# Performance work log

Measured on AMD Instinct MI355X. Metric: run time of the kernel, lower is better.

## Reference

```python
import jax, jax.numpy as jnp
import numpy as np

N, E = 20000, 100000          # nodes, edges
H = 64                        # node_hidden_dim (== node_input_dim)
EIN, EH = 16, 128             # edge_input_dim, edge_hidden_dim
STEPS = 3                     # num_steps


def setup_inputs() -> dict:
    key = jax.random.key(0)
    ks = jax.random.split(key, 10)
    s = 0.05
    return {
        "node_features": jax.random.normal(ks[0], (N, H), jnp.float32),
        "edge_attr": jax.random.normal(ks[1], (E, EIN), jnp.float32),
        "edge_index": jax.random.randint(ks[2], (2, E), 0, N),
        # mp_input: Linear(H, H)
        "mp_w": jax.random.normal(ks[3], (H, H), jnp.float32) * s,
        "mp_b": jnp.zeros((H,), jnp.float32),
        # message_layer: Linear(2H, H)
        "msg_w": jax.random.normal(ks[4], (H, 2 * H), jnp.float32) * s,
        "msg_b": jnp.zeros((H,), jnp.float32),
        # edge network: Linear(EIN, EH) -> ReLU -> Linear(EH, H*H)
        "e1_w": jax.random.normal(ks[5], (EH, EIN), jnp.float32) * s,
        "e1_b": jnp.zeros((EH,), jnp.float32),
        "e2_w": jax.random.normal(ks[6], (H * H, EH), jnp.float32) * s,
        "e2_b": jnp.zeros((H * H,), jnp.float32),
        # NNConv root weight and bias
        "root": jax.random.normal(ks[7], (H, H), jnp.float32) * s,
        "conv_b": jnp.zeros((H,), jnp.float32),
    }


def reference(node_features, edge_attr, edge_index,
              mp_w, mp_b, msg_w, msg_b,
              e1_w, e1_b, e2_w, e2_b, root, conv_b):
    src, dst = edge_index[0], edge_index[1]
    out = jax.nn.relu(node_features @ mp_w.T + mp_b)  # [N, H]
    # Edge-conditioned weight matrices; edge_attr is constant across steps so
    # the edge MLP output is identical each step -> compute once (same math).
    W_e = (jax.nn.relu(edge_attr @ e1_w.T + e1_b) @ e2_w.T + e2_b).reshape(E, H, H)
    for _ in range(STEPS):
        # gather src features, per-edge matmul, scatter-add to dst
        msgs = jnp.einsum('ei,eio->eo', out[src], W_e)          # [E, H]
        agg = jax.ops.segment_sum(msgs, dst, num_segments=N)    # [N, H]
        m = jax.nn.relu(agg + out @ root + conv_b)              # NNConv + ReLU
        out = jnp.concatenate([m, out], axis=1) @ msg_w.T + msg_b
    return out + node_features
```

## Files before the change

kernel.cpp:

```cpp
#include <hip/hip_runtime.h>

#define N_ 20000
#define E_ 100000

typedef __attribute__((ext_vector_type(8))) short short8;
typedef __attribute__((ext_vector_type(4))) float f32x4;

__device__ __forceinline__ unsigned short f2bf(float f) {
  union { float f; unsigned u; } v; v.f = f;
  unsigned r = v.u + 0x7fffu + ((v.u >> 16) & 1u);
  return (unsigned short)(r >> 16);
}
__device__ __forceinline__ float bf2f(unsigned short h) {
  union { unsigned u; float f; } v; v.u = ((unsigned)h) << 16;
  return v.f;
}
__device__ __forceinline__ short8 pack8(float4 a, float4 b) {
  short8 v;
  v[0] = (short)f2bf(a.x); v[1] = (short)f2bf(a.y);
  v[2] = (short)f2bf(a.z); v[3] = (short)f2bf(a.w);
  v[4] = (short)f2bf(b.x); v[5] = (short)f2bf(b.y);
  v[6] = (short)f2bf(b.z); v[7] = (short)f2bf(b.w);
  return v;
}

__global__ __launch_bounds__(256) void k_h2(const float* __restrict__ ea,
                                            const float* __restrict__ e1w,
                                            const float* __restrict__ e1b,
                                            unsigned short* __restrict__ h2) {
  int t = threadIdx.x, w = t >> 6, l = t & 63, g = l >> 4, lm = l & 15;
  short8 bf[8];
#pragma unroll
  for (int cf = 0; cf < 8; ++cf) {
    int c = cf * 16 + lm;
    short8 v = {0, 0, 0, 0, 0, 0, 0, 0};
    if (g < 2) {
      const float4* wp = (const float4*)(e1w + c * 16 + g * 8);
      v = pack8(wp[0], wp[1]);
    } else if (g == 2) {
      v[0] = (short)f2bf(e1b[c]);
    }
    bf[cf] = v;
  }
  const f32x4 z = {0.f, 0.f, 0.f, 0.f};
  for (int tile = 0; tile < 4; ++tile) {
    int e0 = blockIdx.x * 256 + tile * 64 + w * 16;
    if (e0 >= E_) break;
    int er = e0 + lm; if (er >= E_) er = E_ - 1;
    short8 a = {0, 0, 0, 0, 0, 0, 0, 0};
    if (g < 2) {
      const float4* ap = (const float4*)(ea + er * 16 + g * 8);
      a = pack8(ap[0], ap[1]);
    } else if (g == 2) {
      a[0] = (short)0x3F80;
    }
#pragma unroll
    for (int cf = 0; cf < 8; ++cf) {
      f32x4 acc = __builtin_amdgcn_mfma_f32_16x16x32_bf16(a, bf[cf], z, 0, 0, 0);
#pragma unroll
      for (int r = 0; r < 4; ++r) {
        int e = e0 + g * 4 + r;
        if (e < E_) h2[(size_t)e * 128 + cf * 16 + lm] = f2bf(fmaxf(acc[r], 0.f));
      }
    }
  }
}

__global__ __launch_bounds__(256) void k_prep_bf(const float* __restrict__ e2w,
                                                 unsigned short* __restrict__ Af) {
  int tid = blockIdx.x * 256 + threadIdx.x;
  int l = tid & 63, kf = (tid >> 6) & 3, ct = tid >> 8;
  int gq = l >> 4, lm = l & 15;
  const float* src = e2w + (ct * 16 + lm) * 128 + kf * 32 + gq * 8;
  short8 v = pack8(*(const float4*)src, *(const float4*)(src + 4));
  *(short8*)((short*)Af + (size_t)tid * 8) = v;
}

__global__ __launch_bounds__(256) void k_node_in(const float* __restrict__ nfm,
                                                 const float* __restrict__ mpw,
                                                 const float* __restrict__ mpb,
                                                 const float* __restrict__ e2b,
                                                 float* __restrict__ outc,
                                                 float* __restrict__ yc) {
  __shared__ float wT[64 * 65];
  __shared__ float xr[4 * 65];
  __shared__ float nr[4 * 65];
  int t = threadIdx.x;
  for (int idx = t; idx < 4096; idx += 256) {
    int o = idx >> 6, i = idx & 63;
    wT[i * 65 + o] = mpw[idx];
  }
  __syncthreads();
  int nl = t >> 6, o = t & 63;
  for (int it = 0; it < 4; ++it) {
    int n = blockIdx.x * 16 + it * 4 + nl;
    xr[nl * 65 + o] = nfm[n * 64 + o];
    __syncthreads();
    float acc = mpb[o];
#pragma unroll 8
    for (int i = 0; i < 64; ++i) acc += xr[nl * 65 + i] * wT[i * 65 + o];
    float m = fmaxf(acc, 0.f);
    outc[n * 64 + o] = m;
    nr[nl * 65 + o] = m;
    __syncthreads();
    float yv = 0.f;
#pragma unroll 8
    for (int j = 0; j < 64; ++j) yv += nr[nl * 65 + j] * e2b[j * 64 + o];
    yc[n * 64 + o] = yv;
    __syncthreads();
  }
}

__global__ void k_zero(float* __restrict__ p, int n) {
  int i = blockIdx.x * 256 + threadIdx.x;
  if (i < n) p[i] = 0.f;
}

__global__ __launch_bounds__(512, 4) void k_msgs(const float* __restrict__ x,
                                                 const float* __restrict__ y,
                                                 const unsigned short* __restrict__ h2,
                                                 const unsigned short* __restrict__ Af,
                                                 const int* __restrict__ ei,
                                                 float* __restrict__ agg) {
  __shared__ unsigned short xg[64 * 130];
  __shared__ unsigned short pm[8 * 32 * 66];
  __shared__ int sidx[128];
  __shared__ int didx[128];
  int t = threadIdx.x, w = t >> 6, l = t & 63;
  int s = w >> 2, q = w & 3;
  int gq = l >> 4, lm = l & 15;
  int e0 = blockIdx.x * 128;
  if (t < 128) {
    int e = e0 + t;
    sidx[t] = (e < E_) ? ei[e] : 0;
    didx[t] = (e < E_) ? ei[E_ + e] : -1;
  }
  __syncthreads();
  short8 hf[2][4];
#pragma unroll
  for (int ef = 0; ef < 2; ++ef) {
    int e = e0 + q * 32 + ef * 16 + lm;
    if (e >= E_) e = E_ - 1;
    const short8* hp = (const short8*)(h2 + (size_t)e * 128 + gq * 8);
    hf[ef][0] = hp[0]; hf[ef][1] = hp[4]; hf[ef][2] = hp[8]; hf[ef][3] = hp[12];
  }
  {
    int e = t >> 2, seg = t & 3;
    const float* xr = x + (size_t)sidx[e] * 64 + seg * 16;
    float4 v0 = *(const float4*)(xr + 0);
    float4 v1 = *(const float4*)(xr + 4);
    float4 v2 = *(const float4*)(xr + 8);
    float4 v3 = *(const float4*)(xr + 12);
    int ib = seg * 16;
    xg[(ib + 0) * 130 + e] = f2bf(v0.x);  xg[(ib + 1) * 130 + e] = f2bf(v0.y);
    xg[(ib + 2) * 130 + e] = f2bf(v0.z);  xg[(ib + 3) * 130 + e] = f2bf(v0.w);
    xg[(ib + 4) * 130 + e] = f2bf(v1.x);  xg[(ib + 5) * 130 + e] = f2bf(v1.y);
    xg[(ib + 6) * 130 + e] = f2bf(v1.z);  xg[(ib + 7) * 130 + e] = f2bf(v1.w);
    xg[(ib + 8) * 130 + e] = f2bf(v2.x);  xg[(ib + 9) * 130 + e] = f2bf(v2.y);
    xg[(ib + 10) * 130 + e] = f2bf(v2.z); xg[(ib + 11) * 130 + e] = f2bf(v2.w);
    xg[(ib + 12) * 130 + e] = f2bf(v3.x); xg[(ib + 13) * 130 + e] = f2bf(v3.y);
    xg[(ib + 14) * 130 + e] = f2bf(v3.z); xg[(ib + 15) * 130 + e] = f2bf(v3.w);
  }
  __syncthreads();

  f32x4 macc[2][4];
#pragma unroll
  for (int ef = 0; ef < 2; ++ef)
#pragma unroll
    for (int oq = 0; oq < 4; ++oq) macc[ef][oq] = f32x4{0.f, 0.f, 0.f, 0.f};
  const f32x4 z = {0.f, 0.f, 0.f, 0.f};
  const short8* As = (const short8*)Af;

  for (int il = 0; il < 32; ++il) {
    int i = s * 32 + il;
    float xs0 = bf2f(xg[i * 130 + q * 32 + lm]);
    float xs1 = bf2f(xg[i * 130 + q * 32 + 16 + lm]);
#pragma unroll
    for (int oq = 0; oq < 4; ++oq) {
      int ct = i * 4 + oq;
      const short8* ap = As + (size_t)ct * 256 + l;
      short8 a0 = ap[0];
      short8 a1 = ap[64];
      short8 a2 = ap[128];
      short8 a3 = ap[192];
      f32x4 d0, d1;
      d0 = __builtin_amdgcn_mfma_f32_16x16x32_bf16(a0, hf[0][0], z, 0, 0, 0);
      d1 = __builtin_amdgcn_mfma_f32_16x16x32_bf16(a0, hf[1][0], z, 0, 0, 0);
      d0 = __builtin_amdgcn_mfma_f32_16x16x32_bf16(a1, hf[0][1], d0, 0, 0, 0);
      d1 = __builtin_amdgcn_mfma_f32_16x16x32_bf16(a1, hf[1][1], d1, 0, 0, 0);
      d0 = __builtin_amdgcn_mfma_f32_16x16x32_bf16(a2, hf[0][2], d0, 0, 0, 0);
      d1 = __builtin_amdgcn_mfma_f32_16x16x32_bf16(a2, hf[1][2], d1, 0, 0, 0);
      d0 = __builtin_amdgcn_mfma_f32_16x16x32_bf16(a3, hf[0][3], d0, 0, 0, 0);
      d1 = __builtin_amdgcn_mfma_f32_16x16x32_bf16(a3, hf[1][3], d1, 0, 0, 0);
      macc[0][oq] += xs0 * d0;
      macc[1][oq] += xs1 * d1;
    }
  }
  unsigned short* pw = pm + w * 2112;
#pragma unroll
  for (int ef = 0; ef < 2; ++ef)
#pragma unroll
    for (int oq = 0; oq < 4; ++oq)
#pragma unroll
      for (int r = 0; r < 4; ++r)
        pw[(ef * 16 + lm) * 66 + oq * 16 + gq * 4 + r] = f2bf(macc[ef][oq][r]);
  __syncthreads();
  for (int it = 0; it < 16; ++it) {
    int idx = it * 512 + t;
    int e = idx >> 6, o = idx & 63;
    int d = didx[e];
    if (d >= 0) {
      int qe = e >> 5, el = e & 31;
      float v = bf2f(pm[qe * 2112 + el * 66 + o]) + bf2f(pm[(4 + qe) * 2112 + el * 66 + o]);
      v += y[(size_t)sidx[e] * 64 + o];
      atomicAdd(agg + (size_t)d * 64 + o, v);
    }
  }
}

__global__ __launch_bounds__(256) void k_update(const float* __restrict__ outc,
                                                float* __restrict__ agg,
                                                const float* __restrict__ root,
                                                const float* __restrict__ convb,
                                                const float* __restrict__ msgw,
                                                const float* __restrict__ msgb,
                                                const float* __restrict__ e2b,
                                                const float* __restrict__ nfm,
                                                int last,
                                                float* __restrict__ outn,
                                                float* __restrict__ yn,
                                                float* __restrict__ dout) {
  __shared__ float wT[128 * 65];
  __shared__ float xr[4 * 65];
  __shared__ float mr[4 * 65];
  __shared__ float nr[4 * 65];
  int t = threadIdx.x;
  for (int idx = t; idx < 8192; idx += 256) {
    int o = idx >> 7, j = idx & 127;
    wT[j * 65 + o] = msgw[idx];
  }
  __syncthreads();
  int nl = t >> 6, o = t & 63;
  for (int it = 0; it < 4; ++it) {
    int n = blockIdx.x * 16 + it * 4 + nl;
    xr[nl * 65 + o] = outc[n * 64 + o];
    __syncthreads();
    float acc = agg[n * 64 + o] + convb[o];
    agg[n * 64 + o] = 0.f;
#pragma unroll 8
    for (int i = 0; i < 64; ++i) acc += xr[nl * 65 + i] * root[i * 64 + o];
    float m = fmaxf(acc, 0.f);
    mr[nl * 65 + o] = m;
    __syncthreads();
    float o2 = msgb[o];
#pragma unroll 8
    for (int j = 0; j < 64; ++j)
      o2 += mr[nl * 65 + j] * wT[j * 65 + o] + xr[nl * 65 + j] * wT[(64 + j) * 65 + o];
    nr[nl * 65 + o] = o2;
    __syncthreads();
    if (last) {
      dout[n * 64 + o] = o2 + nfm[n * 64 + o];
    } else {
      float yv = 0.f;
#pragma unroll 8
      for (int j = 0; j < 64; ++j) yv += nr[nl * 65 + j] * e2b[j * 64 + o];
      outn[n * 64 + o] = o2;
      yn[n * 64 + o] = yv;
    }
    __syncthreads();
  }
}

extern "C" void kernel_launch(void* const* d_in, const int* in_sizes, int n_in,
                              void* d_out, int out_size, void* d_ws, size_t ws_size,
                              hipStream_t stream) {
  const float* nfm  = (const float*)d_in[0];
  const float* ea   = (const float*)d_in[1];
  const int*   ei   = (const int*)d_in[2];
  const float* mpw  = (const float*)d_in[3];
  const float* mpb  = (const float*)d_in[4];
  const float* msgw = (const float*)d_in[5];
  const float* msgb = (const float*)d_in[6];
  const float* e1w  = (const float*)d_in[7];
  const float* e1b  = (const float*)d_in[8];
  const float* e2w  = (const float*)d_in[9];
  const float* e2b  = (const float*)d_in[10];
  const float* root = (const float*)d_in[11];
  const float* convb= (const float*)d_in[12];
  float* out = (float*)d_out;

  char* ws = (char*)d_ws;
  unsigned short* h2 = (unsigned short*)ws; ws += (size_t)E_ * 128 * 2;
  unsigned short* Af = (unsigned short*)ws; ws += (size_t)4096 * 128 * 2;
  float* outa = (float*)ws; ws += (size_t)N_ * 64 * 4;
  float* ya   = (float*)ws; ws += (size_t)N_ * 64 * 4;
  float* outb = (float*)ws; ws += (size_t)N_ * 64 * 4;
  float* yb   = (float*)ws; ws += (size_t)N_ * 64 * 4;
  float* agg  = (float*)ws; ws += (size_t)N_ * 64 * 4;

  hipLaunchKernelGGL(k_prep_bf, dim3(256), dim3(256), 0, stream, e2w, Af);
  hipLaunchKernelGGL(k_zero, dim3((N_ * 64 + 255) / 256), dim3(256), 0, stream, agg, N_ * 64);
  hipLaunchKernelGGL(k_h2, dim3((E_ + 255) / 256), dim3(256), 0, stream, ea, e1w, e1b, h2);
  hipLaunchKernelGGL(k_node_in, dim3(N_ / 16), dim3(256), 0, stream, nfm, mpw, mpb, e2b, outa, ya);

  float* oc = outa; float* yc = ya; float* on = outb; float* yv = yb;
  for (int s = 0; s < 3; ++s) {
    hipLaunchKernelGGL(k_msgs, dim3((E_ + 127) / 128), dim3(512), 0, stream, oc, yc, h2, Af, ei, agg);
    hipLaunchKernelGGL(k_update, dim3(N_ / 16), dim3(256), 0, stream, oc, agg, root, convb,
                       msgw, msgb, e2b, nfm, (s == 2) ? 1 : 0, on, yv, out);
    float* tp;
    tp = oc; oc = on; on = tp;
    tp = yc; yc = yv; yv = tp;
  }
}
```

Baseline: 694.2 us.

## Restructure edge-message kernel so each warp reuses weight fragments across all edges

The message kernel drops from 512 to 256 threads. Each wave now owns a slice of output columns and K-half and loops over all 128 edges of the block, so every loaded bf16 weight fragment of the edge-network matrix feeds eight edge tiles instead of two. That cuts global/L2 weight traffic per block. Gathered source features are kept in fp32 in a shared pool that is reused for the partial-sum buffer. The node kernels process 64 nodes per block instead of 16 to amortize the per-block weight transpose into shared memory, at the cost of fewer blocks and bounds checks.

```diff
diff --git a/kernel.cpp b/kernel.cpp
--- a/kernel.cpp
+++ b/kernel.cpp
@@ -92,21 +92,23 @@
   }
   __syncthreads();
   int nl = t >> 6, o = t & 63;
-  for (int it = 0; it < 4; ++it) {
-    int n = blockIdx.x * 16 + it * 4 + nl;
-    xr[nl * 65 + o] = nfm[n * 64 + o];
+  for (int it = 0; it < 16; ++it) {
+    int n = blockIdx.x * 64 + it * 4 + nl;
+    bool ok = n < N_;
+    int nc = ok ? n : N_ - 1;
+    xr[nl * 65 + o] = nfm[(size_t)nc * 64 + o];
     __syncthreads();
     float acc = mpb[o];
 #pragma unroll 8
     for (int i = 0; i < 64; ++i) acc += xr[nl * 65 + i] * wT[i * 65 + o];
     float m = fmaxf(acc, 0.f);
-    outc[n * 64 + o] = m;
+    if (ok) outc[(size_t)n * 64 + o] = m;
     nr[nl * 65 + o] = m;
     __syncthreads();
     float yv = 0.f;
 #pragma unroll 8
     for (int j = 0; j < 64; ++j) yv += nr[nl * 65 + j] * e2b[j * 64 + o];
-    yc[n * 64 + o] = yv;
+    if (ok) yc[(size_t)n * 64 + o] = yv;
     __syncthreads();
   }
 }
@@ -116,18 +118,17 @@
   if (i < n) p[i] = 0.f;
 }
 
-__global__ __launch_bounds__(512, 4) void k_msgs(const float* __restrict__ x,
+__global__ __launch_bounds__(256, 3) void k_msgs(const float* __restrict__ x,
                                                  const float* __restrict__ y,
                                                  const unsigned short* __restrict__ h2,
                                                  const unsigned short* __restrict__ Af,
                                                  const int* __restrict__ ei,
                                                  float* __restrict__ agg) {
-  __shared__ unsigned short xg[64 * 130];
-  __shared__ unsigned short pm[8 * 32 * 66];
+  __shared__ __align__(16) unsigned char POOL[33792];
   __shared__ int sidx[128];
   __shared__ int didx[128];
   int t = threadIdx.x, w = t >> 6, l = t & 63;
-  int s = w >> 2, q = w & 3;
+  int op = w >> 1, kh = w & 1;
   int gq = l >> 4, lm = l & 15;
   int e0 = blockIdx.x * 128;
   if (t < 128) {
@@ -136,82 +137,78 @@
     didx[t] = (e < E_) ? ei[E_ + e] : -1;
   }
   __syncthreads();
-  short8 hf[2][4];
-#pragma unroll
-  for (int ef = 0; ef < 2; ++ef) {
-    int e = e0 + q * 32 + ef * 16 + lm;
+  int kb = 2 * kh;
+  short8 hf[8][2];
+#pragma unroll
+  for (int ef = 0; ef < 8; ++ef) {
+    int e = e0 + ef * 16 + lm;
     if (e >= E_) e = E_ - 1;
     const short8* hp = (const short8*)(h2 + (size_t)e * 128 + gq * 8);
-    hf[ef][0] = hp[0]; hf[ef][1] = hp[4]; hf[ef][2] = hp[8]; hf[ef][3] = hp[12];
-  }
+    hf[ef][0] = hp[(kb + 0) * 4];
+    hf[ef][1] = hp[(kb + 1) * 4];
+  }
+  float* xg = (float*)POOL;
   {
-    int e = t >> 2, seg = t & 3;
-    const float* xr = x + (size_t)sidx[e] * 64 + seg * 16;
-    float4 v0 = *(const float4*)(xr + 0);
-    float4 v1 = *(const float4*)(xr + 4);
-    float4 v2 = *(const float4*)(xr + 8);
-    float4 v3 = *(const float4*)(xr + 12);
-    int ib = seg * 16;
-    xg[(ib + 0) * 130 + e] = f2bf(v0.x);  xg[(ib + 1) * 130 + e] = f2bf(v0.y);
-    xg[(ib + 2) * 130 + e] = f2bf(v0.z);  xg[(ib + 3) * 130 + e] = f2bf(v0.w);
-    xg[(ib + 4) * 130 + e] = f2bf(v1.x);  xg[(ib + 5) * 130 + e] = f2bf(v1.y);
-    xg[(ib + 6) * 130 + e] = f2bf(v1.z);  xg[(ib + 7) * 130 + e] = f2bf(v1.w);
-    xg[(ib + 8) * 130 + e] = f2bf(v2.x);  xg[(ib + 9) * 130 + e] = f2bf(v2.y);
-    xg[(ib + 10) * 130 + e] = f2bf(v2.z); xg[(ib + 11) * 130 + e] = f2bf(v2.w);
-    xg[(ib + 12) * 130 + e] = f2bf(v3.x); xg[(ib + 13) * 130 + e] = f2bf(v3.y);
-    xg[(ib + 14) * 130 + e] = f2bf(v3.z); xg[(ib + 15) * 130 + e] = f2bf(v3.w);
-  }
-  __syncthreads();
-
-  f32x4 macc[2][4];
-#pragma unroll
-  for (int ef = 0; ef < 2; ++ef)
-#pragma unroll
-    for (int oq = 0; oq < 4; ++oq) macc[ef][oq] = f32x4{0.f, 0.f, 0.f, 0.f};
+    int e = t >> 1, h = t & 1;
+    const float* xr = x + (size_t)sidx[e] * 64 + h * 32;
+#pragma unroll
+    for (int q = 0; q < 8; ++q) {
+      float4 v = *(const float4*)(xr + q * 4);
+      int ib = h * 32 + q * 4;
+      xg[(ib + 0) * 132 + e] = v.x;
+      xg[(ib + 1) * 132 + e] = v.y;
+      xg[(ib + 2) * 132 + e] = v.z;
+      xg[(ib + 3) * 132 + e] = v.w;
+    }
+  }
+  __syncthreads();
+
+  f32x4 macc[8][2];
+#pragma unroll
+  for (int ef = 0; ef < 8; ++ef) {
+    macc[ef][0] = f32x4{0.f, 0.f, 0.f, 0.f};
+    macc[ef][1] = f32x4{0.f, 0.f, 0.f, 0.f};
+  }
   const f32x4 z = {0.f, 0.f, 0.f, 0.f};
   const short8* As = (const short8*)Af;
-
-  for (int il = 0; il < 32; ++il) {
-    int i = s * 32 + il;
-    float xs0 = bf2f(xg[i * 130 + q * 32 + lm]);
-    float xs1 = bf2f(xg[i * 130 + q * 32 + 16 + lm]);
-#pragma unroll
-    for (int oq = 0; oq < 4; ++oq) {
-      int ct = i * 4 + oq;
-      const short8* ap = As + (size_t)ct * 256 + l;
-      short8 a0 = ap[0];
-      short8 a1 = ap[64];
-      short8 a2 = ap[128];
-      short8 a3 = ap[192];
+  int fb = 2 * op;
+
+  for (int i = 0; i < 64; ++i) {
+    int ct0 = i * 4 + fb;
+    const short8* p0 = As + (size_t)(ct0 * 4 + kb) * 64 + l;
+    short8 w00 = p0[0];
+    short8 w01 = p0[64];
+    short8 w10 = p0[256];
+    short8 w11 = p0[320];
+#pragma unroll
+    for (int ef = 0; ef < 8; ++ef) {
+      float xs = xg[i * 132 + ef * 16 + lm];
       f32x4 d0, d1;
-      d0 = __builtin_amdgcn_mfma_f32_16x16x32_bf16(a0, hf[0][0], z, 0, 0, 0);
-      d1 = __builtin_amdgcn_mfma_f32_16x16x32_bf16(a0, hf[1][0], z, 0, 0, 0);
-      d0 = __builtin_amdgcn_mfma_f32_16x16x32_bf16(a1, hf[0][1], d0, 0, 0, 0);
-      d1 = __builtin_amdgcn_mfma_f32_16x16x32_bf16(a1, hf[1][1], d1, 0, 0, 0);
-      d0 = __builtin_amdgcn_mfma_f32_16x16x32_bf16(a2, hf[0][2], d0, 0, 0, 0);
-      d1 = __builtin_amdgcn_mfma_f32_16x16x32_bf16(a2, hf[1][2], d1, 0, 0, 0);
-      d0 = __builtin_amdgcn_mfma_f32_16x16x32_bf16(a3, hf[0][3], d0, 0, 0, 0);
-      d1 = __builtin_amdgcn_mfma_f32_16x16x32_bf16(a3, hf[1][3], d1, 0, 0, 0);
-      macc[0][oq] += xs0 * d0;
-      macc[1][oq] += xs1 * d1;
-    }
-  }
-  unsigned short* pw = pm + w * 2112;
-#pragma unroll
-  for (int ef = 0; ef < 2; ++ef)
-#pragma unroll
-    for (int oq = 0; oq < 4; ++oq)
+      d0 = __builtin_amdgcn_mfma_f32_16x16x32_bf16(w00, hf[ef][0], z, 0, 0, 0);
+      d1 = __builtin_amdgcn_mfma_f32_16x16x32_bf16(w10, hf[ef][0], z, 0, 0, 0);
+      d0 = __builtin_amdgcn_mfma_f32_16x16x32_bf16(w01, hf[ef][1], d0, 0, 0, 0);
+      d1 = __builtin_amdgcn_mfma_f32_16x16x32_bf16(w11, hf[ef][1], d1, 0, 0, 0);
+      macc[ef][0] += xs * d0;
+      macc[ef][1] += xs * d1;
+    }
+  }
+  __syncthreads();
+  unsigned short* pm = (unsigned short*)POOL;
+#pragma unroll
+  for (int ef = 0; ef < 8; ++ef)
+#pragma unroll
+    for (int oql = 0; oql < 2; ++oql)
 #pragma unroll
       for (int r = 0; r < 4; ++r)
-        pw[(ef * 16 + lm) * 66 + oq * 16 + gq * 4 + r] = f2bf(macc[ef][oq][r]);
-  __syncthreads();
-  for (int it = 0; it < 16; ++it) {
-    int idx = it * 512 + t;
+        pm[kh * 8448 + (ef * 16 + lm) * 66 + op * 32 + oql * 16 + gq * 4 + r] =
+            f2bf(macc[ef][oql][r]);
+  __syncthreads();
+  for (int it = 0; it < 32; ++it) {
+    int idx = it * 256 + t;
     int e = idx >> 6, o = idx & 63;
     int d = didx[e];
     if (d >= 0) {
-      int qe = e >> 5, el = e & 31;
-      float v = bf2f(pm[qe * 2112 + el * 66 + o]) + bf2f(pm[(4 + qe) * 2112 + el * 66 + o]);
+      float v = bf2f(pm[e * 66 + o]) + bf2f(pm[8448 + e * 66 + o]);
       v += y[(size_t)sidx[e] * 64 + o];
       atomicAdd(agg + (size_t)d * 64 + o, v);
     }
@@ -241,12 +238,14 @@
   }
   __syncthreads();
   int nl = t >> 6, o = t & 63;
-  for (int it = 0; it < 4; ++it) {
-    int n = blockIdx.x * 16 + it * 4 + nl;
-    xr[nl * 65 + o] = outc[n * 64 + o];
-    __syncthreads();
-    float acc = agg[n * 64 + o] + convb[o];
-    agg[n * 64 + o] = 0.f;
+  for (int it = 0; it < 16; ++it) {
+    int n = blockIdx.x * 64 + it * 4 + nl;
+    bool ok = n < N_;
+    int nc = ok ? n : N_ - 1;
+    xr[nl * 65 + o] = outc[(size_t)nc * 64 + o];
+    __syncthreads();
+    float acc = agg[(size_t)nc * 64 + o] + convb[o];
+    if (ok) agg[(size_t)n * 64 + o] = 0.f;
 #pragma unroll 8
     for (int i = 0; i < 64; ++i) acc += xr[nl * 65 + i] * root[i * 64 + o];
     float m = fmaxf(acc, 0.f);
@@ -259,13 +258,15 @@
     nr[nl * 65 + o] = o2;
     __syncthreads();
     if (last) {
-      dout[n * 64 + o] = o2 + nfm[n * 64 + o];
+      if (ok) dout[(size_t)n * 64 + o] = o2 + nfm[(size_t)n * 64 + o];
     } else {
       float yv = 0.f;
 #pragma unroll 8
       for (int j = 0; j < 64; ++j) yv += nr[nl * 65 + j] * e2b[j * 64 + o];
-      outn[n * 64 + o] = o2;
-      yn[n * 64 + o] = yv;
+      if (ok) {
+        outn[(size_t)n * 64 + o] = o2;
+        yn[(size_t)n * 64 + o] = yv;
+      }
     }
     __syncthreads();
   }
@@ -301,12 +302,12 @@
   hipLaunchKernelGGL(k_prep_bf, dim3(256), dim3(256), 0, stream, e2w, Af);
   hipLaunchKernelGGL(k_zero, dim3((N_ * 64 + 255) / 256), dim3(256), 0, stream, agg, N_ * 64);
   hipLaunchKernelGGL(k_h2, dim3((E_ + 255) / 256), dim3(256), 0, stream, ea, e1w, e1b, h2);
-  hipLaunchKernelGGL(k_node_in, dim3(N_ / 16), dim3(256), 0, stream, nfm, mpw, mpb, e2b, outa, ya);
+  hipLaunchKernelGGL(k_node_in, dim3((N_ + 63) / 64), dim3(256), 0, stream, nfm, mpw, mpb, e2b, outa, ya);
 
   float* oc = outa; float* yc = ya; float* on = outb; float* yv = yb;
   for (int s = 0; s < 3; ++s) {
-    hipLaunchKernelGGL(k_msgs, dim3((E_ + 127) / 128), dim3(512), 0, stream, oc, yc, h2, Af, ei, agg);
-    hipLaunchKernelGGL(k_update, dim3(N_ / 16), dim3(256), 0, stream, oc, agg, root, convb,
+    hipLaunchKernelGGL(k_msgs, dim3((E_ + 127) / 128), dim3(256), 0, stream, oc, yc, h2, Af, ei, agg);
+    hipLaunchKernelGGL(k_update, dim3((N_ + 63) / 64), dim3(256), 0, stream, oc, agg, root, convb,
                        msgw, msgb, e2b, nfm, (s == 2) ? 1 : 0, on, yv, out);
     float* tp;
     tp = oc; oc = on; on = tp;
```

Result: slower. 763.3 us (+10.0%).
